# Performance work log

Measured on AMD Instinct MI355X. Metric: run time of the kernel, lower is better.

Reference implementation:

```python
import jax, jax.numpy as jnp
import numpy as np

B, C, H, W = 4, 256, 64, 64
CI = 3
TEMPERATURE = 0.0001 * 5
EPS = 2.220446049250313e-16  # sys.float_info.epsilon


def _nearest_up4(x):
    # nn.Upsample(scale_factor=4, mode='nearest'): [B,C,H,W] -> [B,C,4H,4W]
    return jnp.repeat(jnp.repeat(x, 4, axis=2), 4, axis=3)


def _avg_pool2(x):
    # AvgPool2d(kernel=2, stride=2, pad=0)
    b, c, h, w = x.shape
    return x.reshape(b, c, h // 2, 2, w // 2, 2).mean(axis=(3, 5))


def _center_norm(feats):
    # subtract per-channel spatial mean, then L2-normalize over channels per position
    b, c, h, w = feats.shape
    t = feats.reshape(b, c, h * w)
    t = t - t.mean(axis=-1, keepdims=True)
    n = jnp.linalg.norm(t, axis=1, keepdims=True) + EPS
    return t / n  # [B,C,HW]


def setup_inputs() -> dict:
    key = jax.random.key(0)
    k1, k2, k3 = jax.random.split(key, 3)
    return {
        "x_feats": jax.random.normal(k1, (B, C, H, W), jnp.float32),
        "y_feats": jax.random.normal(k2, (B, C, H, W), jnp.float32),
        "y_img": jax.random.uniform(k3, (B, CI, 4 * H, 4 * W), jnp.float32),
    }


def reference(x_feats, y_feats, y_img):
    b, c, h, w = x_feats.shape
    hw = h * w
    theta = _center_norm(x_feats)  # [B,C,HW]
    phi = _center_norm(y_feats)    # [B,C,HW]
    f = jnp.einsum('bcm,bcn->bmn', theta, phi)  # dense correlation [B,HW,HW]
    loss_feat_pair = jnp.mean(jnp.abs(theta - phi))  # F.l1_loss(theta, phi)
    # WTA_scale_weight == 1 -> WTA branch bypassed, just temperature scaling
    f_wta = f / TEMPERATURE
    f_div_c = jax.nn.softmax(f_wta, axis=-1)  # [B,HW,HW]
    # warped features: f_div_C @ y_feats^T
    b_lab = y_feats.reshape(b, c, hw)
    y = jnp.einsum('bmn,bcn->bcm', f_div_c, b_lab).reshape(b, c, h, w)
    # soft-argmax coordinates
    xc = (jnp.arange(hw) % w).astype(x_feats.dtype)   # [HW]
    yc = (jnp.arange(hw) // w).astype(x_feats.dtype)  # [HW]
    coords_x = f_div_c @ xc  # [B,HW]
    coords_y = f_div_c @ yc  # [B,HW]
    coords1 = jnp.stack([coords_x, coords_y], axis=1).reshape(b, 2, h, w)
    coords0 = jnp.stack([xc, yc], axis=0).reshape(1, 2, h, w)
    flow = _nearest_up4(coords1 - coords0)  # [B,2,4H,4W]
    # image warping branch (y_img is not None)
    yi = _avg_pool2(_avg_pool2(y_img))  # [B,CI,H,W]
    ci = yi.shape[1]
    yi_flat = yi.reshape(b, ci, hw)
    y_img_attn = jnp.einsum('bmn,bcn->bmc', f_div_c, yi_flat)  # [B,HW,CI]
    f_div_c_v = jax.nn.softmax(jnp.swapaxes(f_wta, 1, 2), axis=-1)
    y_img_cyc = jnp.einsum('bmn,bnc->bcm', f_div_c_v, y_img_attn).reshape(b, ci, h, w)
    y_img_out = jnp.swapaxes(y_img_attn, 1, 2).reshape(b, ci, h, w)
    return (y, flow, _nearest_up4(y_img_out), _nearest_up4(y_img_cyc), loss_feat_pair)
```

## Files before the change

kernel.cpp:

```cpp
#include <hip/hip_runtime.h>
#include <math.h>

#define HW   4096
#define NCH  256
#define NB   4

constexpr float TEMP  = (float)(0.0001 * 5.0);
constexpr float INV_T = 1.0f / TEMP;
constexpr float EPSN  = 2.220446049250313e-16f;

typedef __attribute__((ext_vector_type(8))) _Float16 f16x8;
typedef __attribute__((ext_vector_type(4))) _Float16 f16x4;
typedef __attribute__((ext_vector_type(4))) float    f32x4;

constexpr size_t OFF_YT    = 0;
constexpr size_t OFF_YI    = OFF_YT    + (size_t)NB*HW*NCH;
constexpr size_t OFF_MEAN  = OFF_YI    + (size_t)NB*3*HW;
constexpr size_t OFF_RNORM = OFF_MEAN  + (size_t)2*NB*NCH;
constexpr size_t OFF_NSQP  = OFF_RNORM + (size_t)2*NB*HW;
constexpr size_t OFF_F     = OFF_NSQP  + (size_t)2*NB*8*HW;
constexpr size_t OFF_YP    = OFF_F     + (size_t)HW*HW;
constexpr size_t OFF_ROWP  = OFF_YP;
constexpr size_t OFF_COLP  = OFF_YP + (size_t)32*7*HW;
constexpr size_t OFF_RMAX  = OFF_YP    + (size_t)8*NCH*HW;
constexpr size_t OFF_RSUM  = OFF_RMAX  + HW;
constexpr size_t OFF_CMAX  = OFF_RSUM  + HW;
constexpr size_t OFF_RMB   = OFF_CMAX  + HW;
constexpr size_t OFF_COORD = OFF_RMB   + (size_t)32*HW;
constexpr size_t OFF_ATTN  = OFF_COORD + (size_t)NB*2*HW;
constexpr size_t OFF_CYC   = OFF_ATTN  + (size_t)NB*HW*3;
constexpr size_t OFF_CYCP  = OFF_CYC   + (size_t)NB*3*HW;
constexpr size_t OFF_LOSSP = OFF_CYCP  + (size_t)32*4*HW;
constexpr size_t OFF_F16   = OFF_LOSSP + 1024;

constexpr size_t OUT_Y    = 0;
constexpr size_t OUT_FLOW = (size_t)NB*NCH*HW;
constexpr size_t OUT_IMG  = OUT_FLOW + (size_t)NB*2*256*256;
constexpr size_t OUT_CYCO = OUT_IMG  + (size_t)NB*3*256*256;
constexpr size_t OUT_LOSS = OUT_CYCO + (size_t)NB*3*256*256;

__device__ __forceinline__ void gload16(const void* g, void* l) {
    __builtin_amdgcn_global_load_lds(
        (const __attribute__((address_space(1))) unsigned int*)g,
        (__attribute__((address_space(3))) unsigned int*)l, 16, 0, 0);
}

__global__ void mean_kernel(const float* __restrict__ xf, const float* __restrict__ yf,
                            float* __restrict__ means) {
    const float* src = (blockIdx.y == 0 ? xf : yf) + (size_t)blockIdx.x * HW;
    float s = 0.f;
    for (int i = threadIdx.x; i < HW; i += 256) s += src[i];
    __shared__ float red[256];
    red[threadIdx.x] = s; __syncthreads();
    for (int st = 128; st > 0; st >>= 1) {
        if (threadIdx.x < st) red[threadIdx.x] += red[threadIdx.x + st];
        __syncthreads();
    }
    if (threadIdx.x == 0) means[blockIdx.y * (NB*NCH) + blockIdx.x] = red[0] * (1.0f / HW);
}

__global__ void nsq_combine_kernel(const float* __restrict__ part, float* __restrict__ rnorms,
                                   int b) {
    int t = blockIdx.y;
    int m = blockIdx.x * 256 + threadIdx.x;
    const float* p = part + ((size_t)t*NB + b) * 8 * HW + m;
    float s = 0.f;
    for (int k = 0; k < 8; ++k) s += p[(size_t)k * HW];
    rnorms[((size_t)t*NB + b) * HW + m] = 1.0f / (sqrtf(s) + EPSN);
}

__global__ void ycast_kernel(const float* __restrict__ yf, _Float16* __restrict__ yf16) {
    size_t i = ((size_t)blockIdx.x * 256 + threadIdx.x) * 8;
    const float4* s = (const float4*)(yf + i);
    float4 v0 = s[0], v1 = s[1];
    f16x8 o;
    o[0]=(_Float16)v0.x; o[1]=(_Float16)v0.y; o[2]=(_Float16)v0.z; o[3]=(_Float16)v0.w;
    o[4]=(_Float16)v1.x; o[5]=(_Float16)v1.y; o[6]=(_Float16)v1.z; o[7]=(_Float16)v1.w;
    *(f16x8*)(yf16 + i) = o;
}

__global__ void prep_kernel(const float* __restrict__ xf, const float* __restrict__ yf,
                            const float* __restrict__ means,
                            _Float16* __restrict__ th, _Float16* __restrict__ tl,
                            _Float16* __restrict__ ph, _Float16* __restrict__ pl,
                            float* __restrict__ nsqp, int b) {
    __shared__ float tile[32][33];
    __shared__ float sqr[8][33];
    int t = blockIdx.z;
    int c0 = blockIdx.x * 32, m0 = blockIdx.y * 32;
    const float* src = (t == 0 ? xf : yf) + (size_t)b * NCH * HW;
    const float* mn  = means + t * (NB*NCH) + b * NCH;
    int tx = threadIdx.x & 31, ty = threadIdx.x >> 5;
    float sq = 0.f;
    for (int i = ty; i < 32; i += 8) {
        float v = src[(size_t)(c0 + i) * HW + m0 + tx] - mn[c0 + i];
        tile[i][tx] = v;
        sq += v * v;
    }
    sqr[ty][tx] = sq;
    __syncthreads();
    _Float16* H = (t == 0 ? th : ph);
    _Float16* L = (t == 0 ? tl : pl);
    for (int i = ty; i < 32; i += 8) {
        float v = tile[tx][i];
        _Float16 h = (_Float16)v;
        _Float16 l = (_Float16)(v - (float)h);
        H[(size_t)(m0 + i)*NCH + c0 + tx] = h;
        L[(size_t)(m0 + i)*NCH + c0 + tx] = l;
    }
    if (ty == 0) {
        float s = 0.f;
        #pragma unroll
        for (int k = 0; k < 8; ++k) s += sqr[k][tx];
        nsqp[(((size_t)t*NB + b) * 8 + blockIdx.x) * HW + m0 + tx] = s;
    }
}

__global__ void avgpool_kernel(const float* __restrict__ yimg, float* __restrict__ yi) {
    size_t idx = (size_t)blockIdx.x * 256 + threadIdx.x;
    int m  = (int)(idx & (HW - 1));
    int bc = (int)(idx >> 12);
    int h = m >> 6, w = m & 63;
    const float* p = yimg + (size_t)bc * 65536 + (size_t)(h*4) * 256 + w*4;
    float s = 0.f;
    #pragma unroll
    for (int dy = 0; dy < 4; ++dy) {
        #pragma unroll
        for (int dx = 0; dx < 4; ++dx) s += p[dy*256 + dx];
    }
    yi[idx] = s * (1.0f/16.0f);
}

__global__ __launch_bounds__(512) void gemm_f_kernel(
        const _Float16* __restrict__ th, const _Float16* __restrict__ tl,
        const _Float16* __restrict__ ph, const _Float16* __restrict__ pl,
        const float* __restrict__ rnorms, const float* __restrict__ yi,
        _Float16* __restrict__ zh, float* __restrict__ rowp, float* __restrict__ colp,
        float* __restrict__ rmb, int b) {
    __shared__ char lds[2][4][8192];
    int tid  = threadIdx.x;
    int lane = tid & 63;
    int w = tid >> 6;
    int wm = w >> 2;
    int wn = w & 3;
    int m0 = blockIdx.y * 128, n0 = blockIdx.x * 128;

    int o0 = tid * 16;
    int r0 = o0 >> 6, s0 = (o0 >> 4) & 3, g0 = s0 ^ ((r0 >> 1) & 3);
    size_t ga0 = (size_t)(n0 + r0)*NCH + g0*8;
    size_t gb0 = (size_t)(m0 + r0)*NCH + g0*8;

    int fra = wm*64 + (lane & 15);
    int frb = wn*32 + (lane & 15);
    int ks  = lane >> 4;

    auto STAGE = [&](int buf, int k0) {
        gload16(ph + ga0 + k0, &lds[buf][0][o0]);
        gload16(pl + ga0 + k0, &lds[buf][1][o0]);
        gload16(th + gb0 + k0, &lds[buf][2][o0]);
        gload16(tl + gb0 + k0, &lds[buf][3][o0]);
    };

    f32x4 acc[4][2];
    #pragma unroll
    for (int i = 0; i < 4; ++i)
        #pragma unroll
        for (int j = 0; j < 2; ++j) acc[i][j] = (f32x4){0.f, 0.f, 0.f, 0.f};

    STAGE(0, 0);
    __syncthreads();
    int cur = 0;
    for (int kt = 0; kt < 8; ++kt) {
        if (kt < 7) STAGE(cur ^ 1, (kt + 1) * 32);

        f16x8 ah[4], al[4], bh[2], bl[2];
        #pragma unroll
        for (int i = 0; i < 4; ++i) {
            int rowa = fra + i*16;
            int offa = rowa*64 + ((ks ^ ((rowa >> 1) & 3)) << 4);
            ah[i] = *(const f16x8*)&lds[cur][0][offa];
            al[i] = *(const f16x8*)&lds[cur][1][offa];
        }
        #pragma unroll
        for (int j = 0; j < 2; ++j) {
            int rowb = frb + j*16;
            int offb = rowb*64 + ((ks ^ ((rowb >> 1) & 3)) << 4);
            bh[j] = *(const f16x8*)&lds[cur][2][offb];
            bl[j] = *(const f16x8*)&lds[cur][3][offb];
        }
        __builtin_amdgcn_s_setprio(1);
        #pragma unroll
        for (int i = 0; i < 4; ++i)
            #pragma unroll
            for (int j = 0; j < 2; ++j) {
                acc[i][j] = __builtin_amdgcn_mfma_f32_16x16x32_f16(ah[i], bh[j], acc[i][j], 0, 0, 0);
                acc[i][j] = __builtin_amdgcn_mfma_f32_16x16x32_f16(ah[i], bl[j], acc[i][j], 0, 0, 0);
                acc[i][j] = __builtin_amdgcn_mfma_f32_16x16x32_f16(al[i], bh[j], acc[i][j], 0, 0, 0);
            }
        __builtin_amdgcn_s_setprio(0);
        __syncthreads();
        cur ^= 1;
    }

    const float* rnx = rnorms + (size_t)b * HW;
    const float* rny = rnorms + (size_t)(NB + b) * HW;
    int mg[2];  float rxv[2];
    #pragma unroll
    for (int j = 0; j < 2; ++j) {
        mg[j] = m0 + wn*32 + j*16 + (lane & 15);
        rxv[j] = rnx[mg[j]];
    }
    int nl0 = wm*64 + (lane >> 4)*4;
    #pragma unroll
    for (int i = 0; i < 4; ++i)
        #pragma unroll
        for (int r = 0; r < 4; ++r) {
            float ry = rny[n0 + nl0 + i*16 + r];
            #pragma unroll
            for (int j = 0; j < 2; ++j) acc[i][j][r] *= rxv[j] * ry;
        }

    float* S     = (float*)&lds[0][0][0];
    float* rowm  = S;
    float* sums6 = S + 256;
    float* colm  = S + 1792;

    #pragma unroll
    for (int j = 0; j < 2; ++j) {
        float v = acc[0][j][0];
        #pragma unroll
        for (int i = 0; i < 4; ++i)
            #pragma unroll
            for (int r = 0; r < 4; ++r) v = fmaxf(v, acc[i][j][r]);
        v = fmaxf(v, __shfl_xor(v, 16));
        v = fmaxf(v, __shfl_xor(v, 32));
        if (lane < 16) rowm[wm*128 + wn*32 + j*16 + lane] = v;
    }
    #pragma unroll
    for (int i = 0; i < 4; ++i)
        #pragma unroll
        for (int r = 0; r < 4; ++r) {
            float v = fmaxf(acc[i][0][r], acc[i][1][r]);
            #pragma unroll
            for (int d = 1; d < 16; d <<= 1) v = fmaxf(v, __shfl_xor(v, d));
            if ((lane & 15) == 0) colm[wn*128 + nl0 + i*16 + r] = v;
        }
    __syncthreads();

    float bm[2];
    #pragma unroll
    for (int j = 0; j < 2; ++j) {
        int ml = wn*32 + j*16 + (lane & 15);
        bm[j] = fmaxf(rowm[ml], rowm[128 + ml]);
    }
    float a6[2][6];
    #pragma unroll
    for (int j = 0; j < 2; ++j)
        #pragma unroll
        for (int q = 0; q < 6; ++q) a6[j][q] = 0.f;
    const float* yib = yi + (size_t)b * 3 * HW;
    #pragma unroll
    for (int i = 0; i < 4; ++i) {
        f16x4 zq[2];
        #pragma unroll
        for (int r = 0; r < 4; ++r) {
            int ng = n0 + nl0 + i*16 + r;
            float xc = (float)(ng & 63), yc = (float)(ng >> 6);
            float y0 = yib[ng], y1 = yib[HW + ng], y2 = yib[2*HW + ng];
            #pragma unroll
            for (int j = 0; j < 2; ++j) {
                float z = (acc[i][j][r] - bm[j]) * INV_T;
                float e = __expf(z);
                zq[j][r] = (_Float16)z;
                a6[j][0] += e;      a6[j][1] += e*xc; a6[j][2] += e*yc;
                a6[j][3] += e*y0;   a6[j][4] += e*y1; a6[j][5] += e*y2;
            }
        }
        #pragma unroll
        for (int j = 0; j < 2; ++j)
            *(f16x4*)&zh[(size_t)mg[j]*HW + n0 + nl0 + i*16] = zq[j];
    }
    #pragma unroll
    for (int j = 0; j < 2; ++j)
        #pragma unroll
        for (int q = 0; q < 6; ++q) {
            float v = a6[j][q];
            v += __shfl_xor(v, 16);
            v += __shfl_xor(v, 32);
            if (lane < 16) sums6[(wm*128 + wn*32 + j*16 + lane)*6 + q] = v;
        }
    __syncthreads();

    if (tid < 128) {
        int ml = tid;
        float m2 = fmaxf(rowm[ml], rowm[128 + ml]);
        rowp[((size_t)blockIdx.x*7 + 0)*HW + m0 + ml] = m2;
        rmb[(size_t)blockIdx.x*HW + m0 + ml] = m2;
        #pragma unroll
        for (int q = 0; q < 6; ++q)
            rowp[((size_t)blockIdx.x*7 + 1 + q)*HW + m0 + ml] =
                sums6[ml*6 + q] + sums6[(128 + ml)*6 + q];
    } else if (tid < 256) {
        int nl = tid - 128;
        float c2 = fmaxf(fmaxf(colm[nl], colm[128 + nl]),
                         fmaxf(colm[256 + nl], colm[384 + nl]));
        colp[(size_t)blockIdx.y*HW + n0 + nl] = c2;
    }
}

__global__ void rowcol_combine_kernel(const float* __restrict__ rowp,
        const float* __restrict__ colp,
        float* __restrict__ rmax, float* __restrict__ rsuminv,
        float* __restrict__ coords, float* __restrict__ attn,
        float* __restrict__ cmax, int b) {
    int idx = blockIdx.x * 256 + threadIdx.x;
    if (blockIdx.y == 0) {
        int m = idx;
        float gm = -3.0e38f;
        for (int t = 0; t < 32; ++t) gm = fmaxf(gm, rowp[((size_t)t*7)*HW + m]);
        float S=0, CX=0, CY=0, A0=0, A1=0, A2=0;
        for (int t = 0; t < 32; ++t) {
            const float* p = rowp + (size_t)t*7*HW + m;
            float wgt = __expf((p[0] - gm) * INV_T);
            S  += p[1*HW] * wgt; CX += p[2*HW] * wgt; CY += p[3*HW] * wgt;
            A0 += p[4*HW] * wgt; A1 += p[5*HW] * wgt; A2 += p[6*HW] * wgt;
        }
        float inv = 1.0f / S;
        rmax[m] = gm; rsuminv[m] = inv;
        coords[((size_t)b*2 + 0)*HW + m] = CX * inv;
        coords[((size_t)b*2 + 1)*HW + m] = CY * inv;
        attn[((size_t)b*HW + m)*3 + 0] = A0 * inv;
        attn[((size_t)b*HW + m)*3 + 1] = A1 * inv;
        attn[((size_t)b*HW + m)*3 + 2] = A2 * inv;
    } else {
        int n = idx;
        float gm = -3.0e38f;
        for (int t = 0; t < 32; ++t) gm = fmaxf(gm, colp[(size_t)t*HW + n]);
        cmax[n] = gm;
    }
}

__global__ __launch_bounds__(512) void gemm_y_kernel(const _Float16* __restrict__ zh,
        const float* __restrict__ rmax, const float* __restrict__ rmb,
        const _Float16* __restrict__ yf16, _Float16* __restrict__ yph, int b) {
    __shared__ __align__(16) char ldsA[4096];
    __shared__ __align__(16) char ldsB[16384];
    int tid  = threadIdx.x;
    int lane = tid & 63;
    int w = tid >> 6, wm = w >> 2, wn = w & 3;
    int m0 = blockIdx.x * 64;
    int ks = blockIdx.y;
    const _Float16* Yb = yf16 + (size_t)b * NCH * HW;

    int ar = tid >> 3, kc = tid & 7;
    int aslot = kc >> 1, ahalf = kc & 1;
    int aoff = ar*64 + ((aslot ^ ((ar >> 1) & 3)) << 4) + ahalf*8;
    float gm = rmax[m0 + ar];
    const _Float16* zrow = zh + (size_t)(m0 + ar)*HW + kc*4;
    const float* rmbm = rmb + (m0 + ar);

    int o0 = tid*16, o1 = o0 + 8192;
    int br0 = o0 >> 6, bs0 = (o0 >> 4) & 3, bg0 = bs0 ^ ((br0 >> 1) & 3);
    int br1 = o1 >> 6, bs1 = (o1 >> 4) & 3, bg1 = bs1 ^ ((br1 >> 1) & 3);
    size_t gb0 = (size_t)br0*HW + bg0*8;
    size_t gb1 = (size_t)br1*HW + bg1*8;

    int fra = wm*32 + (lane & 15);
    int frb = wn*64 + (lane & 15);
    int kslot = lane >> 4;

    f32x4 acc[2][4];
    #pragma unroll
    for (int i = 0; i < 2; ++i)
        #pragma unroll
        for (int j = 0; j < 4; ++j) acc[i][j] = (f32x4){0.f, 0.f, 0.f, 0.f};

    float corrf = 0.f;
    for (int k0 = ks*1024; k0 < ks*1024 + 1024; k0 += 32) {
        gload16(Yb + gb0 + k0, &ldsB[o0]);
        gload16(Yb + gb1 + k0, &ldsB[o1]);
        {
            if ((k0 & 127) == 0)
                corrf = __expf((rmbm[(size_t)(k0 >> 7)*HW] - gm) * INV_T);
            f16x4 zv = *(const f16x4*)(zrow + k0);
            f16x4 pk;
            pk[0] = (_Float16)(__expf((float)zv[0]) * corrf);
            pk[1] = (_Float16)(__expf((float)zv[1]) * corrf);
            pk[2] = (_Float16)(__expf((float)zv[2]) * corrf);
            pk[3] = (_Float16)(__expf((float)zv[3]) * corrf);
            *(f16x4*)&ldsA[aoff] = pk;
        }
        __syncthreads();

        f16x8 af[2], bf[4];
        #pragma unroll
        for (int i = 0; i < 2; ++i) {
            int rowa = fra + i*16;
            af[i] = *(const f16x8*)&ldsA[rowa*64 + ((kslot ^ ((rowa >> 1) & 3)) << 4)];
        }
        #pragma unroll
        for (int j = 0; j < 4; ++j) {
            int rowb = frb + j*16;
            bf[j] = *(const f16x8*)&ldsB[rowb*64 + ((kslot ^ ((rowb >> 1) & 3)) << 4)];
        }
        __builtin_amdgcn_s_setprio(1);
        #pragma unroll
        for (int i = 0; i < 2; ++i)
            #pragma unroll
            for (int j = 0; j < 4; ++j)
                acc[i][j] = __builtin_amdgcn_mfma_f32_16x16x32_f16(af[i], bf[j], acc[i][j], 0, 0, 0);
        __builtin_amdgcn_s_setprio(0);
        __syncthreads();
    }

    #pragma unroll
    for (int i = 0; i < 2; ++i) {
        int m = m0 + wm*32 + i*16 + (lane >> 4) * 4;
        #pragma unroll
        for (int j = 0; j < 4; ++j) {
            int c = wn*64 + j*16 + (lane & 15);
            f16x4 v;
            #pragma unroll
            for (int r = 0; r < 4; ++r) v[r] = (_Float16)acc[i][j][r];
            *(f16x4*)(yph + ((size_t)ks*NCH + c)*HW + m) = v;
        }
    }
}

__global__ void ycombine_kernel(const _Float16* __restrict__ yph, const float* __restrict__ rsuminv,
                                float* __restrict__ out, int b) {
    size_t idx = (size_t)blockIdx.x * 256 + threadIdx.x;
    int m = (int)(idx & (HW - 1));
    float s = 0.f;
    #pragma unroll
    for (int k = 0; k < 4; ++k) s += (float)yph[(size_t)k*NCH*HW + idx];
    out[OUT_Y + (size_t)b*NCH*HW + idx] = s * rsuminv[m];
}

__global__ __launch_bounds__(256) void cyc_partial_kernel(const _Float16* __restrict__ zh,
        const float* __restrict__ cmax, const float* __restrict__ rmb,
        const float* __restrict__ attn, float* __restrict__ part, int b) {
    __shared__ float at[128*3];
    __shared__ float bmL[2][128];
    int i  = blockIdx.x * 256 + threadIdx.x;
    int j0 = blockIdx.y * 128;
    for (int k = threadIdx.x; k < 384; k += 256)
        at[k] = attn[((size_t)b*HW + j0)*3 + k];
    {
        int k = threadIdx.x;
        bmL[k >> 7][k & 127] = rmb[((size_t)(blockIdx.x*2 + (k >> 7)))*HW + j0 + (k & 127)];
    }
    __syncthreads();
    float cm = cmax[i];
    int tl = threadIdx.x >> 7;
    float a0=0, a1=0, a2=0, a3=0;
    for (int jj = 0; jj < 128; ++jj) {
        float z = (float)zh[(size_t)(j0+jj)*HW + i];
        float e = __expf(z + (bmL[tl][jj] - cm) * INV_T);
        a0 = fmaf(e, at[jj*3+0], a0);
        a1 = fmaf(e, at[jj*3+1], a1);
        a2 = fmaf(e, at[jj*3+2], a2);
        a3 += e;
    }
    part[((size_t)blockIdx.y*4 + 0)*HW + i] = a0;
    part[((size_t)blockIdx.y*4 + 1)*HW + i] = a1;
    part[((size_t)blockIdx.y*4 + 2)*HW + i] = a2;
    part[((size_t)blockIdx.y*4 + 3)*HW + i] = a3;
}

__global__ void cyc_combine_kernel(const float* __restrict__ part,
                                   float* __restrict__ cyc, int b) {
    int i = blockIdx.x * 256 + threadIdx.x;
    int c = blockIdx.y;
    float s = 0.f, den = 0.f;
    for (int k = 0; k < 32; ++k) {
        s   += part[((size_t)k*4 + c)*HW + i];
        den += part[((size_t)k*4 + 3)*HW + i];
    }
    cyc[((size_t)b*3 + c)*HW + i] = s / den;
}

__global__ void flow_kernel(const float* __restrict__ coords, float* __restrict__ out) {
    size_t idx = (size_t)blockIdx.x * 256 + threadIdx.x;
    int x4 = (int)(idx & 255);
    int y4 = (int)((idx >> 8) & 255);
    int ch = (int)((idx >> 16) & 1);
    int b  = (int)(idx >> 17);
    int w = x4 >> 2, h = y4 >> 2;
    int m = h*64 + w;
    float c1 = coords[((size_t)b*2 + ch)*HW + m];
    float c0 = (ch == 0) ? (float)w : (float)h;
    out[OUT_FLOW + idx] = c1 - c0;
}

__global__ void imgout_kernel(const float* __restrict__ attn, const float* __restrict__ cyc,
                              float* __restrict__ out) {
    size_t idx = (size_t)blockIdx.x * 256 + threadIdx.x;
    int x4 = (int)(idx & 255);
    int y4 = (int)((idx >> 8) & 255);
    int rest = (int)(idx >> 16);
    int ch = rest % 3, b = rest / 3;
    int m = (y4 >> 2)*64 + (x4 >> 2);
    out[OUT_IMG  + idx] = attn[((size_t)b*HW + m)*3 + ch];
    out[OUT_CYCO + idx] = cyc[((size_t)b*3 + ch)*HW + m];
}

__global__ void loss_partial_kernel(const float* __restrict__ xf, const float* __restrict__ yf,
                                    const float* __restrict__ means, const float* __restrict__ rnorms,
                                    float* __restrict__ part) {
    __shared__ float red[256];
    size_t base = (size_t)blockIdx.x * 4096;
    float s = 0.f;
    for (int k = 0; k < 16; ++k) {
        size_t id = base + (size_t)k*256 + threadIdx.x;
        int m  = (int)(id & (HW - 1));
        int bc = (int)(id >> 12);
        int b  = bc >> 8;
        float th = (xf[id] - means[bc])          * rnorms[(size_t)b*HW + m];
        float ph = (yf[id] - means[NB*NCH + bc]) * rnorms[(size_t)(NB + b)*HW + m];
        s += fabsf(th - ph);
    }
    red[threadIdx.x] = s; __syncthreads();
    for (int st = 128; st > 0; st >>= 1) {
        if (threadIdx.x < st) red[threadIdx.x] += red[threadIdx.x + st];
        __syncthreads();
    }
    if (threadIdx.x == 0) part[blockIdx.x] = red[0];
}

__global__ void loss_final_kernel(const float* __restrict__ part, float* __restrict__ out) {
    __shared__ float red[256];
    float s = 0.f;
    for (int k = threadIdx.x; k < 1024; k += 256) s += part[k];
    red[threadIdx.x] = s; __syncthreads();
    for (int st = 128; st > 0; st >>= 1) {
        if (threadIdx.x < st) red[threadIdx.x] += red[threadIdx.x + st];
        __syncthreads();
    }
    if (threadIdx.x == 0) out[OUT_LOSS] = red[0] * (1.0f / 4194304.0f);
}

extern "C" void kernel_launch(void* const* d_in, const int* in_sizes, int n_in,
                              void* d_out, int out_size, void* d_ws, size_t ws_size,
                              hipStream_t stream) {
    (void)in_sizes; (void)n_in; (void)out_size; (void)ws_size;
    const float* xf   = (const float*)d_in[0];
    const float* yf   = (const float*)d_in[1];
    const float* yimg = (const float*)d_in[2];
    float* out = (float*)d_out;
    float* ws  = (float*)d_ws;

    _Float16* yf16 = (_Float16*)(ws + OFF_YT);
    float* yi      = ws + OFF_YI;
    float* means   = ws + OFF_MEAN;
    float* rnorms  = ws + OFF_RNORM;
    float* nsqp    = ws + OFF_NSQP;
    _Float16* zh   = (_Float16*)(ws + OFF_F);
    _Float16* yph  = (_Float16*)(ws + OFF_YP);
    float* rowp    = ws + OFF_ROWP;
    float* colp    = ws + OFF_COLP;
    float* rmax    = ws + OFF_RMAX;
    float* rsuminv = ws + OFF_RSUM;
    float* cmax    = ws + OFF_CMAX;
    float* rmb     = ws + OFF_RMB;
    float* coords  = ws + OFF_COORD;
    float* attn    = ws + OFF_ATTN;
    float* cyc     = ws + OFF_CYC;
    float* cycp    = ws + OFF_CYCP;
    float* lossp   = ws + OFF_LOSSP;
    _Float16* th = (_Float16*)(ws + OFF_F16);
    _Float16* tl = th + (size_t)HW*NCH;
    _Float16* ph = tl + (size_t)HW*NCH;
    _Float16* pl = ph + (size_t)HW*NCH;

    mean_kernel        <<<dim3(NB*NCH, 2),   256, 0, stream>>>(xf, yf, means);
    ycast_kernel       <<<2048,              256, 0, stream>>>(yf, yf16);
    avgpool_kernel     <<<NB*3*HW/256,       256, 0, stream>>>(yimg, yi);

    for (int b = 0; b < NB; ++b) {
        prep_kernel          <<<dim3(8, 128, 2), 256, 0, stream>>>(xf, yf, means, th, tl, ph, pl,
                                                                   nsqp, b);
        nsq_combine_kernel   <<<dim3(16, 2),     256, 0, stream>>>(nsqp, rnorms, b);
        gemm_f_kernel        <<<dim3(32, 32),    512, 0, stream>>>(th, tl, ph, pl, rnorms, yi,
                                                                   zh, rowp, colp, rmb, b);
        rowcol_combine_kernel<<<dim3(16, 2),     256, 0, stream>>>(rowp, colp, rmax, rsuminv,
                                                                   coords, attn, cmax, b);
        gemm_y_kernel        <<<dim3(64, 4),     512, 0, stream>>>(zh, rmax, rmb, yf16, yph, b);
        ycombine_kernel      <<<NCH*HW/256,      256, 0, stream>>>(yph, rsuminv, out, b);
        cyc_partial_kernel   <<<dim3(16, 32),    256, 0, stream>>>(zh, cmax, rmb, attn, cycp, b);
        cyc_combine_kernel   <<<dim3(16, 3),     256, 0, stream>>>(cycp, cyc, b);
    }

    flow_kernel        <<<NB*2*65536/256, 256, 0, stream>>>(coords, out);
    imgout_kernel      <<<NB*3*65536/256, 256, 0, stream>>>(attn, cyc, out);
    loss_partial_kernel<<<1024,           256, 0, stream>>>(xf, yf, means, rnorms, lossp);
    loss_final_kernel  <<<1,              256, 0, stream>>>(lossp, out);
}
```

Before: 503.3 us.

## Double-buffer gemm_y LDS tiles and batch combine kernels across the batch

gemm_y_kernel now uses two LDS buffers for the A and B tiles. The next K-slice is staged (async global-to-LDS loads for B, exp-scaled writes for A) while MFMAs run on the current slice, which needs only one barrier per iteration. The per-batch ycombine and cyc_combine launches are moved out of the batch loop into single launches over all four batches. To allow this, the workspace is re-laid out so yph, cycp and rsum hold per-batch slices, with cycp, rowp and colp moved into the unused upper half of the F region. This doubles LDS use per block and now recomputes the row correction exp on every K-step, which may lower occupancy and adds a little extra math.

```diff
diff --git a/kernel.cpp b/kernel.cpp
--- a/kernel.cpp
+++ b/kernel.cpp
@@ -19,18 +19,19 @@
 constexpr size_t OFF_RNORM = OFF_MEAN  + (size_t)2*NB*NCH;
 constexpr size_t OFF_NSQP  = OFF_RNORM + (size_t)2*NB*HW;
 constexpr size_t OFF_F     = OFF_NSQP  + (size_t)2*NB*8*HW;
+constexpr size_t OFF_ZUP   = OFF_F     + (size_t)HW*HW/2;
+constexpr size_t OFF_CYCP  = OFF_ZUP;
+constexpr size_t OFF_ROWP  = OFF_CYCP  + (size_t)NB*32*4*HW;
+constexpr size_t OFF_COLP  = OFF_ROWP  + (size_t)32*7*HW;
 constexpr size_t OFF_YP    = OFF_F     + (size_t)HW*HW;
-constexpr size_t OFF_ROWP  = OFF_YP;
-constexpr size_t OFF_COLP  = OFF_YP + (size_t)32*7*HW;
 constexpr size_t OFF_RMAX  = OFF_YP    + (size_t)8*NCH*HW;
 constexpr size_t OFF_RSUM  = OFF_RMAX  + HW;
-constexpr size_t OFF_CMAX  = OFF_RSUM  + HW;
+constexpr size_t OFF_CMAX  = OFF_RSUM  + (size_t)NB*HW;
 constexpr size_t OFF_RMB   = OFF_CMAX  + HW;
 constexpr size_t OFF_COORD = OFF_RMB   + (size_t)32*HW;
 constexpr size_t OFF_ATTN  = OFF_COORD + (size_t)NB*2*HW;
 constexpr size_t OFF_CYC   = OFF_ATTN  + (size_t)NB*HW*3;
-constexpr size_t OFF_CYCP  = OFF_CYC   + (size_t)NB*3*HW;
-constexpr size_t OFF_LOSSP = OFF_CYCP  + (size_t)32*4*HW;
+constexpr size_t OFF_LOSSP = OFF_CYC   + (size_t)NB*3*HW;
 constexpr size_t OFF_F16   = OFF_LOSSP + 1024;
 
 constexpr size_t OUT_Y    = 0;
@@ -343,8 +344,8 @@
 __global__ __launch_bounds__(512) void gemm_y_kernel(const _Float16* __restrict__ zh,
         const float* __restrict__ rmax, const float* __restrict__ rmb,
         const _Float16* __restrict__ yf16, _Float16* __restrict__ yph, int b) {
-    __shared__ __align__(16) char ldsA[4096];
-    __shared__ __align__(16) char ldsB[16384];
+    __shared__ __align__(16) char ldsA[2][4096];
+    __shared__ __align__(16) char ldsB[2][16384];
     int tid  = threadIdx.x;
     int lane = tid & 63;
     int w = tid >> 6, wm = w >> 2, wn = w & 3;
@@ -369,39 +370,48 @@
     int frb = wn*64 + (lane & 15);
     int kslot = lane >> 4;
 
+    auto STAGEB = [&](int buf, int k0) {
+        gload16(Yb + gb0 + k0, &ldsB[buf][o0]);
+        gload16(Yb + gb1 + k0, &ldsB[buf][o1]);
+    };
+    auto WRITEA = [&](int buf, int k0) {
+        float cf = __expf((rmbm[(size_t)(k0 >> 7)*HW] - gm) * INV_T);
+        f16x4 zv = *(const f16x4*)(zrow + k0);
+        f16x4 pk;
+        pk[0] = (_Float16)(__expf((float)zv[0]) * cf);
+        pk[1] = (_Float16)(__expf((float)zv[1]) * cf);
+        pk[2] = (_Float16)(__expf((float)zv[2]) * cf);
+        pk[3] = (_Float16)(__expf((float)zv[3]) * cf);
+        *(f16x4*)&ldsA[buf][aoff] = pk;
+    };
+
     f32x4 acc[2][4];
     #pragma unroll
     for (int i = 0; i < 2; ++i)
         #pragma unroll
         for (int j = 0; j < 4; ++j) acc[i][j] = (f32x4){0.f, 0.f, 0.f, 0.f};
 
-    float corrf = 0.f;
-    for (int k0 = ks*1024; k0 < ks*1024 + 1024; k0 += 32) {
-        gload16(Yb + gb0 + k0, &ldsB[o0]);
-        gload16(Yb + gb1 + k0, &ldsB[o1]);
-        {
-            if ((k0 & 127) == 0)
-                corrf = __expf((rmbm[(size_t)(k0 >> 7)*HW] - gm) * INV_T);
-            f16x4 zv = *(const f16x4*)(zrow + k0);
-            f16x4 pk;
-            pk[0] = (_Float16)(__expf((float)zv[0]) * corrf);
-            pk[1] = (_Float16)(__expf((float)zv[1]) * corrf);
-            pk[2] = (_Float16)(__expf((float)zv[2]) * corrf);
-            pk[3] = (_Float16)(__expf((float)zv[3]) * corrf);
-            *(f16x4*)&ldsA[aoff] = pk;
-        }
-        __syncthreads();
-
+    int kbase = ks * 1024;
+    WRITEA(0, kbase);
+    STAGEB(0, kbase);
+    __syncthreads();
+    int cur = 0;
+    for (int s = 0; s < 32; ++s) {
+        int k0 = kbase + s*32;
+        if (s < 31) {
+            STAGEB(cur ^ 1, k0 + 32);
+            WRITEA(cur ^ 1, k0 + 32);
+        }
         f16x8 af[2], bf[4];
         #pragma unroll
         for (int i = 0; i < 2; ++i) {
             int rowa = fra + i*16;
-            af[i] = *(const f16x8*)&ldsA[rowa*64 + ((kslot ^ ((rowa >> 1) & 3)) << 4)];
+            af[i] = *(const f16x8*)&ldsA[cur][rowa*64 + ((kslot ^ ((rowa >> 1) & 3)) << 4)];
         }
         #pragma unroll
         for (int j = 0; j < 4; ++j) {
             int rowb = frb + j*16;
-            bf[j] = *(const f16x8*)&ldsB[rowb*64 + ((kslot ^ ((rowb >> 1) & 3)) << 4)];
+            bf[j] = *(const f16x8*)&ldsB[cur][rowb*64 + ((kslot ^ ((rowb >> 1) & 3)) << 4)];
         }
         __builtin_amdgcn_s_setprio(1);
         #pragma unroll
@@ -411,6 +421,7 @@
                 acc[i][j] = __builtin_amdgcn_mfma_f32_16x16x32_f16(af[i], bf[j], acc[i][j], 0, 0, 0);
         __builtin_amdgcn_s_setprio(0);
         __syncthreads();
+        cur ^= 1;
     }
 
     #pragma unroll
@@ -427,14 +438,16 @@
     }
 }
 
-__global__ void ycombine_kernel(const _Float16* __restrict__ yph, const float* __restrict__ rsuminv,
-                                float* __restrict__ out, int b) {
+__global__ void ycombine_kernel(const _Float16* __restrict__ yph, const float* __restrict__ rsum,
+                                float* __restrict__ out) {
+    int b = blockIdx.y;
     size_t idx = (size_t)blockIdx.x * 256 + threadIdx.x;
     int m = (int)(idx & (HW - 1));
+    const _Float16* yb = yph + (size_t)b*4*NCH*HW;
     float s = 0.f;
     #pragma unroll
-    for (int k = 0; k < 4; ++k) s += (float)yph[(size_t)k*NCH*HW + idx];
-    out[OUT_Y + (size_t)b*NCH*HW + idx] = s * rsuminv[m];
+    for (int k = 0; k < 4; ++k) s += (float)yb[(size_t)k*NCH*HW + idx];
+    out[OUT_Y + (size_t)b*NCH*HW + idx] = s * rsum[(size_t)b*HW + m];
 }
 
 __global__ __launch_bounds__(256) void cyc_partial_kernel(const _Float16* __restrict__ zh,
@@ -468,8 +481,9 @@
     part[((size_t)blockIdx.y*4 + 3)*HW + i] = a3;
 }
 
-__global__ void cyc_combine_kernel(const float* __restrict__ part,
-                                   float* __restrict__ cyc, int b) {
+__global__ void cyc_combine_kernel(const float* __restrict__ cycp, float* __restrict__ cyc) {
+    int b = blockIdx.z;
+    const float* part = cycp + (size_t)b*32*4*HW;
     int i = blockIdx.x * 256 + threadIdx.x;
     int c = blockIdx.y;
     float s = 0.f, den = 0.f;
@@ -557,16 +571,16 @@
     float* nsqp    = ws + OFF_NSQP;
     _Float16* zh   = (_Float16*)(ws + OFF_F);
     _Float16* yph  = (_Float16*)(ws + OFF_YP);
+    float* cycp    = ws + OFF_CYCP;
     float* rowp    = ws + OFF_ROWP;
     float* colp    = ws + OFF_COLP;
     float* rmax    = ws + OFF_RMAX;
-    float* rsuminv = ws + OFF_RSUM;
+    float* rsum    = ws + OFF_RSUM;
     float* cmax    = ws + OFF_CMAX;
     float* rmb     = ws + OFF_RMB;
     float* coords  = ws + OFF_COORD;
     float* attn    = ws + OFF_ATTN;
     float* cyc     = ws + OFF_CYC;
-    float* cycp    = ws + OFF_CYCP;
     float* lossp   = ws + OFF_LOSSP;
     _Float16* th = (_Float16*)(ws + OFF_F16);
     _Float16* tl = th + (size_t)HW*NCH;
@@ -583,14 +597,17 @@
         nsq_combine_kernel   <<<dim3(16, 2),     256, 0, stream>>>(nsqp, rnorms, b);
         gemm_f_kernel        <<<dim3(32, 32),    512, 0, stream>>>(th, tl, ph, pl, rnorms, yi,
                                                                    zh, rowp, colp, rmb, b);
-        rowcol_combine_kernel<<<dim3(16, 2),     256, 0, stream>>>(rowp, colp, rmax, rsuminv,
+        rowcol_combine_kernel<<<dim3(16, 2),     256, 0, stream>>>(rowp, colp, rmax,
+                                                                   rsum + (size_t)b*HW,
                                                                    coords, attn, cmax, b);
-        gemm_y_kernel        <<<dim3(64, 4),     512, 0, stream>>>(zh, rmax, rmb, yf16, yph, b);
-        ycombine_kernel      <<<NCH*HW/256,      256, 0, stream>>>(yph, rsuminv, out, b);
-        cyc_partial_kernel   <<<dim3(16, 32),    256, 0, stream>>>(zh, cmax, rmb, attn, cycp, b);
-        cyc_combine_kernel   <<<dim3(16, 3),     256, 0, stream>>>(cycp, cyc, b);
-    }
-
+        gemm_y_kernel        <<<dim3(64, 4),     512, 0, stream>>>(zh, rmax, rmb, yf16,
+                                                                   yph + (size_t)b*4*NCH*HW, b);
+        cyc_partial_kernel   <<<dim3(16, 32),    256, 0, stream>>>(zh, cmax, rmb, attn,
+                                                                   cycp + (size_t)b*32*4*HW, b);
+    }
+
+    ycombine_kernel    <<<dim3(NCH*HW/256, NB), 256, 0, stream>>>(yph, rsum, out);
+    cyc_combine_kernel <<<dim3(16, 3, NB),      256, 0, stream>>>(cycp, cyc);
     flow_kernel        <<<NB*2*65536/256, 256, 0, stream>>>(coords, out);
     imgout_kernel      <<<NB*3*65536/256, 256, 0, stream>>>(attn, cyc, out);
     loss_partial_kernel<<<1024,           256, 0, stream>>>(xf, yf, means, rnorms, lossp);
```

After: 477.7 us. 1.05x faster.
